# Performance work log

Hardware: AMD Instinct MI355X
Metric: run time of the kernel (lower is better)

## Reference

```python
import jax, jax.numpy as jnp
import numpy as np

B, T, H, NH, L = 2, 2048, 1024, 16, 6
D = H // NH          # head dim = 64
FF = 4 * H           # MLP hidden = 4096
EPS = 1e-5           # torch LayerNorm default

CAUSAL = np.tril(np.ones((T, T), dtype=bool))  # [T,T] lower-triangular mask


def _ln(x, g, b):
    m = jnp.mean(x, axis=-1, keepdims=True)
    v = jnp.mean(jnp.square(x - m), axis=-1, keepdims=True)
    return (x - m) * jax.lax.rsqrt(v + EPS) * g + b


def _block(x, p):
    Wq, bq, Wk, bk, Wv, bv, Wp, bp, W1, b1, W2, b2, g1, be1, g2, be2 = p
    mask = jnp.asarray(CAUSAL)
    # qkv projections -> [B, NH, T, D]
    q = (x @ Wq + bq).reshape(B, T, NH, D).transpose(0, 2, 1, 3)
    k = (x @ Wk + bk).reshape(B, T, NH, D).transpose(0, 2, 1, 3)
    v = (x @ Wv + bv).reshape(B, T, NH, D).transpose(0, 2, 1, 3)
    scores = jnp.einsum('bhtd,bhsd->bhts', q, k) / jnp.sqrt(jnp.float32(D))
    scores = jnp.where(mask, scores, -jnp.inf)
    attn = jax.nn.softmax(scores, axis=-1)
    o = jnp.einsum('bhts,bhsd->bhtd', attn, v)
    o = o.transpose(0, 2, 1, 3).reshape(B, T, H) @ Wp + bp
    x = _ln(x + o, g1, be1)            # residual then ln1 (post-LN, as in source)
    h = jax.nn.gelu(x @ W1 + b1, approximate=False)
    x = _ln(x + h @ W2 + b2, g2, be2)  # residual then ln2
    return x


def setup_inputs() -> dict:
    key = jax.random.key(0)
    ks = jax.random.split(key, 8)
    s = 0.02
    w = lambda k, shape: jax.random.normal(k, shape, jnp.float32) * s
    return {
        'x':  jax.random.normal(ks[0], (B, T, H), jnp.float32),
        'Wq': w(ks[1], (L, H, H)),  'bq': jnp.zeros((L, H), jnp.float32),
        'Wk': w(ks[2], (L, H, H)),  'bk': jnp.zeros((L, H), jnp.float32),
        'Wv': w(ks[3], (L, H, H)),  'bv': jnp.zeros((L, H), jnp.float32),
        'Wp': w(ks[4], (L, H, H)),  'bp': jnp.zeros((L, H), jnp.float32),
        'W1': w(ks[5], (L, H, FF)), 'b1': jnp.zeros((L, FF), jnp.float32),
        'W2': w(ks[6], (L, FF, H)), 'b2': jnp.zeros((L, H), jnp.float32),
        'g1': jnp.ones((L, H), jnp.float32),  'be1': jnp.zeros((L, H), jnp.float32),
        'g2': jnp.ones((L, H), jnp.float32),  'be2': jnp.zeros((L, H), jnp.float32),
    }


def reference(x, Wq, bq, Wk, bk, Wv, bv, Wp, bp, W1, b1, W2, b2, g1, be1, g2, be2):
    params = (Wq, bq, Wk, bk, Wv, bv, Wp, bp, W1, b1, W2, b2, g1, be1, g2, be2)
    y, _ = jax.lax.scan(lambda c, p: (_block(c, p), None), x, params)
    return y
```

## Files before the change

### kernel.cpp

```cpp
#include <hip/hip_runtime.h>

constexpr int cB  = 2;
constexpr int cT  = 2048;
constexpr int cH  = 1024;
constexpr int cNH = 16;
constexpr int cFF = 4096;
constexpr int cL  = 6;
constexpr int cM  = cB * cT;

typedef __attribute__((ext_vector_type(8))) short short8;
typedef __attribute__((ext_vector_type(4))) float f32x4;
typedef __attribute__((ext_vector_type(4))) unsigned short u16x4;
typedef unsigned short u16;

__device__ __forceinline__ u16 f2bf(float f) {
  union { float f; unsigned int u; } v; v.f = f;
  unsigned int u = v.u;
  return (u16)((u + 0x7fffu + ((u >> 16) & 1u)) >> 16);
}

__device__ __forceinline__ void glds16(const void* g, void* l) {
  __builtin_amdgcn_global_load_lds(
      (__attribute__((address_space(1))) void*)(unsigned long long)g,
      (__attribute__((address_space(3))) void*)(unsigned int)(unsigned long long)l,
      16, 0, 0);
}

#define EPI_F32 0
#define EPI_GELU 1
#define EPI_QKV 2

template <int EPI>
__global__ __launch_bounds__(512, 2) void gemm256(
    const u16* __restrict__ A,
    const u16* __restrict__ B0, const u16* __restrict__ B1, const u16* __restrict__ B2,
    const float* __restrict__ bias0, const float* __restrict__ bias1, const float* __restrict__ bias2,
    void* __restrict__ out0, void* __restrict__ out1, void* __restrict__ out2, void* __restrict__ out3,
    int M, int N, int K, int ntn)
{
  __shared__ u16 lds[65536];

  const int tid = threadIdx.x;
  const int wave = tid >> 6, lane = tid & 63;
  const int l15 = lane & 15, q4 = lane >> 4;
  const int wm = wave >> 2, wn = wave & 3;
  const int mt = blockIdx.x;
  const int by = blockIdx.y;
  const int mat = by / ntn;
  const int nt = by - mat * ntn;
  const u16* BT = (mat == 0) ? B0 : ((mat == 1) ? B1 : B2);
  const float* bias = (mat == 0) ? bias0 : ((mat == 1) ? bias1 : bias2);
  void* out = (mat == 0) ? out0 : ((mat == 1) ? out1 : out2);

  const int kz = blockIdx.z;
  const int kpc = K / gridDim.z;
  const int kb0 = kz * kpc;
  if (EPI == EPI_F32) {
    void* outs[4] = {out0, out1, out2, out3};
    out = outs[kz];
    if (kz > 0) bias = nullptr;
  }
  const int nkt = kpc >> 5;

  const u16* Ag[2]; const u16* Bg[2];
#pragma unroll
  for (int j = 0; j < 2; ++j) {
    const int d = j * 8192 + tid * 16;
    const int l = d ^ (((d >> 6) & 3) << 4);
    const int srow = l >> 6, skel = (l & 63) >> 1;
    Ag[j] = A  + (size_t)(mt * 256 + srow) * K + kb0 + skel;
    Bg[j] = BT + (size_t)(nt * 256 + srow) * K + kb0 + skel;
  }

  auto stageA = [&](int tt) {
    u16* dst = lds + ((tt & 3) << 14) + (tid << 3);
    glds16(Ag[0] + (tt << 5), dst);
    glds16(Ag[1] + (tt << 5), dst + 4096);
  };
  auto stageB = [&](int tt) {
    u16* dst = lds + ((tt & 3) << 14) + 8192 + (tid << 3);
    glds16(Bg[0] + (tt << 5), dst);
    glds16(Bg[1] + (tt << 5), dst + 4096);
  };

  const int sb = (l15 & 3) << 4;

  f32x4 acc[8][4] = {};
  short8 a[4], b[4];

  stageA(0); stageB(0); stageA(1); stageB(1);
  asm volatile("s_waitcnt vmcnt(4)" ::: "memory");
  __builtin_amdgcn_s_barrier();

  for (int t = 0; t < nkt; ++t) {
    const u16* As = lds + ((t & 3) << 14);
    const u16* Bs = As + 8192;
    const bool pre = (t + 2 < nkt);

#pragma unroll
    for (int nf = 0; nf < 4; ++nf) {
      const int r = wn * 64 + nf * 16 + l15;
      b[nf] = *(const short8*)(Bs + ((((r << 6) + (q4 << 4)) ^ sb) >> 1));
    }
#pragma unroll
    for (int m = 0; m < 4; ++m) {
      const int r = wm * 128 + m * 16 + l15;
      a[m] = *(const short8*)(As + ((((r << 6) + (q4 << 4)) ^ sb) >> 1));
    }
    if (pre) stageA(t + 2);
    __builtin_amdgcn_s_barrier();
    asm volatile("s_waitcnt lgkmcnt(0)" ::: "memory");
    __builtin_amdgcn_sched_barrier(0);
    __builtin_amdgcn_s_setprio(1);
#pragma unroll
    for (int m = 0; m < 4; ++m)
#pragma unroll
      for (int nf = 0; nf < 4; ++nf)
        acc[m][nf] = __builtin_amdgcn_mfma_f32_16x16x32_bf16(a[m], b[nf], acc[m][nf], 0, 0, 0);
    __builtin_amdgcn_s_setprio(0);
    __builtin_amdgcn_s_barrier();

#pragma unroll
    for (int m = 0; m < 4; ++m) {
      const int r = wm * 128 + (m + 4) * 16 + l15;
      a[m] = *(const short8*)(As + ((((r << 6) + (q4 << 4)) ^ sb) >> 1));
    }
    if (pre) stageB(t + 2);
    __builtin_amdgcn_s_barrier();
    asm volatile("s_waitcnt lgkmcnt(0)" ::: "memory");
    __builtin_amdgcn_sched_barrier(0);
    __builtin_amdgcn_s_setprio(1);
#pragma unroll
    for (int m = 0; m < 4; ++m)
#pragma unroll
      for (int nf = 0; nf < 4; ++nf)
        acc[m + 4][nf] = __builtin_amdgcn_mfma_f32_16x16x32_bf16(a[m], b[nf], acc[m + 4][nf], 0, 0, 0);
    __builtin_amdgcn_s_setprio(0);
    if (pre) asm volatile("s_waitcnt vmcnt(4)" ::: "memory");
    else     asm volatile("s_waitcnt vmcnt(0)" ::: "memory");
    __builtin_amdgcn_s_barrier();
  }

  float bj[4];
#pragma unroll
  for (int nf = 0; nf < 4; ++nf)
    bj[nf] = bias ? bias[nt * 256 + wn * 64 + nf * 16 + l15] : 0.0f;

  const float qscale = (EPI == EPI_QKV && mat == 0) ? 0.125f : 1.0f;

#pragma unroll
  for (int mf = 0; mf < 8; ++mf) {
#pragma unroll
    for (int nf = 0; nf < 4; ++nf) {
      const int n = nt * 256 + wn * 64 + nf * 16 + l15;
#pragma unroll
      for (int r = 0; r < 4; ++r) {
        const int m = mt * 256 + wm * 128 + mf * 16 + (q4 << 2) + r;
        float vv = acc[mf][nf][r] + bj[nf];
        if (EPI == EPI_F32) {
          ((float*)out)[(size_t)m * N + n] = vv;
        } else if (EPI == EPI_GELU) {
          float gg = vv * 0.5f * (1.0f + erff(vv * 0.70710678118654752f));
          ((u16*)out)[(size_t)m * N + n] = f2bf(gg);
        } else {
          const int bb = m >> 11, tt = m & (cT - 1);
          const int h = n >> 6, d = n & 63;
          ((u16*)out)[((((size_t)bb * cNH + h) * cT + tt) << 6) + d] = f2bf(vv * qscale);
        }
      }
    }
  }
}

template <int EPI>
__global__ __launch_bounds__(256) void gemm_bt(
    const u16* __restrict__ A,
    const u16* __restrict__ B0, const u16* __restrict__ B1, const u16* __restrict__ B2,
    const float* __restrict__ bias0, const float* __restrict__ bias1, const float* __restrict__ bias2,
    void* __restrict__ out0, void* __restrict__ out1, void* __restrict__ out2, void* __restrict__ out3,
    int M, int N, int K, int ntn)
{
  __shared__ u16 As[128 * 32];
  __shared__ u16 Bs[128 * 32];
  const int tid = threadIdx.x;
  const int wave = tid >> 6;
  const int lane = tid & 63;
  const int l15 = lane & 15;
  const int q4 = lane >> 4;
  const int mt = blockIdx.x;
  const int by = blockIdx.y;
  const int mat = by / ntn;
  const int nt = by - mat * ntn;
  const u16* BT = (mat == 0) ? B0 : ((mat == 1) ? B1 : B2);
  const float* bias = (mat == 0) ? bias0 : ((mat == 1) ? bias1 : bias2);
  void* out = (mat == 0) ? out0 : ((mat == 1) ? out1 : out2);

  const int kz = blockIdx.z;
  const int kpc = K / gridDim.z;
  const int kb0 = kz * kpc, kb1 = kb0 + kpc;
  if (EPI == EPI_F32) {
    void* outs[4] = {out0, out1, out2, out3};
    out = outs[kz];
    if (kz > 0) bias = nullptr;
  }

  const int wr = (wave >> 1) << 6;
  const int wc = (wave & 1) << 6;

  f32x4 acc[4][4] = {};

  const int srow = (wave << 5) + (lane >> 2);
  const int scol = (lane & 3) << 3;
  const u16* Ag = A + (size_t)(mt * 128 + srow) * K + scol;
  const u16* Bg = BT + (size_t)(nt * 128 + srow) * K + scol;
  u16* AsD = As + (wave << 10);
  u16* BsD = Bs + (wave << 10);

  for (int k0 = kb0; k0 < kb1; k0 += 32) {
    glds16(Ag + k0, AsD);
    glds16(Ag + k0 + 16 * K, AsD + 512);
    glds16(Bg + k0, BsD);
    glds16(Bg + k0 + 16 * K, BsD + 512);
    __syncthreads();
    short8 av[4], bv[4];
#pragma unroll
    for (int i = 0; i < 4; ++i)
      av[i] = *(const short8*)(As + ((wr + i * 16 + l15) << 5) + (q4 << 3));
#pragma unroll
    for (int j = 0; j < 4; ++j)
      bv[j] = *(const short8*)(Bs + ((wc + j * 16 + l15) << 5) + (q4 << 3));
#pragma unroll
    for (int i = 0; i < 4; ++i)
#pragma unroll
      for (int j = 0; j < 4; ++j)
        acc[i][j] = __builtin_amdgcn_mfma_f32_16x16x32_bf16(av[i], bv[j], acc[i][j], 0, 0, 0);
    __syncthreads();
  }

  float bj[4];
#pragma unroll
  for (int j = 0; j < 4; ++j) bj[j] = bias ? bias[nt * 128 + wc + j * 16 + l15] : 0.0f;

  const float qscale = (EPI == EPI_QKV && mat == 0) ? 0.125f : 1.0f;

#pragma unroll
  for (int i = 0; i < 4; ++i) {
#pragma unroll
    for (int j = 0; j < 4; ++j) {
      const int n = nt * 128 + wc + j * 16 + l15;
#pragma unroll
      for (int r = 0; r < 4; ++r) {
        const int m = mt * 128 + wr + i * 16 + (q4 << 2) + r;
        float vv = acc[i][j][r] + bj[j];
        if (EPI == EPI_F32) {
          ((float*)out)[(size_t)m * N + n] = vv;
        } else if (EPI == EPI_GELU) {
          float gg = vv * 0.5f * (1.0f + erff(vv * 0.70710678118654752f));
          ((u16*)out)[(size_t)m * N + n] = f2bf(gg);
        } else {
          const int b = m >> 11, t = m & (cT - 1);
          const int h = n >> 6, d = n & 63;
          ((u16*)out)[((((size_t)b * cNH + h) * cT + t) << 6) + d] = f2bf(vv * qscale);
        }
      }
    }
  }
}

__global__ __launch_bounds__(256) void flash_attn(
    const u16* __restrict__ q, const u16* __restrict__ k,
    const u16* __restrict__ v, u16* __restrict__ o)
{
  __shared__ u16 Vt[2][64 * 80];
  __shared__ u16 Pl[8][16 * 80];

  const int tid = threadIdx.x, wave = tid >> 6, lane = tid & 63;
  const int l15 = lane & 15, q4 = lane >> 4;
  const int bx = blockIdx.x;
  const int qtH = 31 - bx;
  const int qtL = bx;
  const int bh = blockIdx.y;
  const u16* qh = q + ((size_t)bh * cT << 6);
  const u16* kh = k + ((size_t)bh * cT << 6);
  const u16* vh = v + ((size_t)bh * cT << 6);

  short8 qfH[2], qfL[2];
#pragma unroll
  for (int kk = 0; kk < 2; ++kk) {
    qfH[kk] = *(const short8*)(qh + (size_t)((qtH << 6) + wave * 16 + l15) * 64 + kk * 32 + q4 * 8);
    qfL[kk] = *(const short8*)(qh + (size_t)((qtL << 6) + wave * 16 + l15) * 64 + kk * 32 + q4 * 8);
  }

  short8 ones;
#pragma unroll
  for (int i = 0; i < 8; ++i) ones[i] = (short)0x3F80;

  uint4 vs0, vs1;
  auto vload = [&](int st) {
    const int s0 = st << 6;
    const u16* src = vh + (size_t)(s0 + lane) * 64 + wave * 8;
    vs0 = *(const uint4*)(src);
    vs1 = *(const uint4*)(src + 32);
  };
  auto vwrite = [&](int buf) {
    u16* Vb = &Vt[buf][0];
    const int s = lane;
#pragma unroll
    for (int rd = 0; rd < 2; ++rd) {
      const int d0 = wave * 8 + rd * 32;
      uint4 vv = rd ? vs1 : vs0;
      Vb[(d0 + 0) * 80 + s] = (u16)(vv.x & 0xffff);
      Vb[(d0 + 1) * 80 + s] = (u16)(vv.x >> 16);
      Vb[(d0 + 2) * 80 + s] = (u16)(vv.y & 0xffff);
      Vb[(d0 + 3) * 80 + s] = (u16)(vv.y >> 16);
      Vb[(d0 + 4) * 80 + s] = (u16)(vv.z & 0xffff);
      Vb[(d0 + 5) * 80 + s] = (u16)(vv.z >> 16);
      Vb[(d0 + 6) * 80 + s] = (u16)(vv.w & 0xffff);
      Vb[(d0 + 7) * 80 + s] = (u16)(vv.w >> 16);
    }
  };

  auto loadK = [&](int st, short8* kf) {
    const int s0 = st << 6;
#pragma unroll
    for (int j = 0; j < 4; ++j)
#pragma unroll
      for (int kk = 0; kk < 2; ++kk)
        kf[j * 2 + kk] = *(const short8*)(kh + (size_t)(s0 + j * 16 + l15) * 64 + kk * 32 + q4 * 8);
  };

  f32x4 oaH[4] = {}, oaL[4] = {};
  f32x4 lsH = {}, lsL = {};

  auto tileQ = [&](int kt, int qt, const short8* qf, const short8* kf,
                   f32x4* oa, f32x4& ls, int buf, u16* pl) {
    f32x4 sa[4];
#pragma unroll
    for (int j = 0; j < 4; ++j) {
      f32x4 zz = {};
      zz = __builtin_amdgcn_mfma_f32_16x16x32_bf16(qf[0], kf[j * 2 + 0], zz, 0, 0, 0);
      zz = __builtin_amdgcn_mfma_f32_16x16x32_bf16(qf[1], kf[j * 2 + 1], zz, 0, 0, 0);
      sa[j] = zz;
    }
    if (kt == qt) {
#pragma unroll
      for (int r = 0; r < 4; ++r) {
        const int trow = wave * 16 + q4 * 4 + r;
#pragma unroll
        for (int j = 0; j < 4; ++j) {
          float pv = (j * 16 + l15 > trow) ? 0.0f : __expf(sa[j][r]);
          pl[(q4 * 4 + r) * 80 + j * 16 + l15] = f2bf(pv);
        }
      }
    } else {
#pragma unroll
      for (int r = 0; r < 4; ++r)
#pragma unroll
        for (int j = 0; j < 4; ++j)
          pl[(q4 * 4 + r) * 80 + j * 16 + l15] = f2bf(__expf(sa[j][r]));
    }
#pragma unroll
    for (int kk = 0; kk < 2; ++kk) {
      short8 pf = *(const short8*)(&pl[l15 * 80 + kk * 32 + q4 * 8]);
      ls = __builtin_amdgcn_mfma_f32_16x16x32_bf16(pf, ones, ls, 0, 0, 0);
#pragma unroll
      for (int jd = 0; jd < 4; ++jd) {
        short8 vf = *(const short8*)(&Vt[buf][(jd * 16 + l15) * 80 + kk * 32 + q4 * 8]);
        oa[jd] = __builtin_amdgcn_mfma_f32_16x16x32_bf16(pf, vf, oa[jd], 0, 0, 0);
      }
    }
  };

  auto tile = [&](int kt, const short8* kf, int buf) {
    tileQ(kt, qtH, qfH, kf, oaH, lsH, buf, &Pl[wave][0]);
    if (kt <= qtL)
      tileQ(kt, qtL, qfL, kf, oaL, lsL, buf, &Pl[wave + 4][0]);
  };

  const int nk = qtH + 1;
  short8 kfA[8], kfB[8];
  vload(0);
  loadK(0, kfA);
  vwrite(0);
  __syncthreads();

  int kt = 0;
  for (; kt + 2 <= nk; kt += 2) {
    vload(kt + 1);
    loadK(kt + 1, kfB);
    tile(kt, kfA, 0);
    vwrite(1);
    __syncthreads();
    if (kt + 2 < nk) { vload(kt + 2); loadK(kt + 2, kfA); }
    tile(kt + 1, kfB, 1);
    if (kt + 2 < nk) vwrite(0);
    __syncthreads();
  }
  if (kt < nk) { tile(kt, kfA, 0); }

  const int b = bh >> 4, h = bh & 15;
#pragma unroll
  for (int r = 0; r < 4; ++r) {
    const int tH = (qtH << 6) + wave * 16 + (q4 << 2) + r;
    const int tL = (qtL << 6) + wave * 16 + (q4 << 2) + r;
    const float invH = 1.0f / lsH[r];
    const float invL = 1.0f / lsL[r];
#pragma unroll
    for (int jd = 0; jd < 4; ++jd) {
      const int d = jd * 16 + l15;
      o[((size_t)(b * cT + tH)) * cH + (h << 6) + d] = f2bf(oaH[jd][r] * invH);
      o[((size_t)(b * cT + tL)) * cH + (h << 6) + d] = f2bf(oaL[jd][r] * invL);
    }
  }
}

template <int NY>
__global__ __launch_bounds__(256) void add_ln_k(
    const float* __restrict__ x,
    const float* __restrict__ y0, const float* __restrict__ y1,
    const float* __restrict__ y2, const float* __restrict__ y3,
    const float* __restrict__ g, const float* __restrict__ be,
    float* __restrict__ xout, u16* __restrict__ xb)
{
  const float* ys[4] = {y0, y1, y2, y3};
  const int row = blockIdx.x;
  const int c = threadIdx.x << 2;
  const size_t base = ((size_t)row << 10) + c;
  f32x4 vv = *(const f32x4*)(x + base);
#pragma unroll
  for (int p = 0; p < NY; ++p) {
    f32x4 yv = *(const f32x4*)(ys[p] + base);
#pragma unroll
    for (int t = 0; t < 4; ++t) vv[t] += yv[t];
  }
  float s1 = vv[0] + vv[1] + vv[2] + vv[3];
  float s2 = vv[0] * vv[0] + vv[1] * vv[1] + vv[2] * vv[2] + vv[3] * vv[3];
#pragma unroll
  for (int off = 1; off < 64; off <<= 1) {
    s1 += __shfl_xor(s1, off);
    s2 += __shfl_xor(s2, off);
  }
  __shared__ float sm[8];
  const int wave = threadIdx.x >> 6, lane = threadIdx.x & 63;
  if (lane == 0) { sm[wave] = s1; sm[wave + 4] = s2; }
  __syncthreads();
  const float S1 = sm[0] + sm[1] + sm[2] + sm[3];
  const float S2 = sm[4] + sm[5] + sm[6] + sm[7];
  const float mean = S1 * (1.0f / cH);
  const float var = S2 * (1.0f / cH) - mean * mean;
  const float rstd = rsqrtf(var + 1e-5f);
  f32x4 gv = *(const f32x4*)(g + c);
  f32x4 bv = *(const f32x4*)(be + c);
  f32x4 ov; u16x4 ob;
#pragma unroll
  for (int t = 0; t < 4; ++t) {
    ov[t] = (vv[t] - mean) * rstd * gv[t] + bv[t];
    ob[t] = f2bf(ov[t]);
  }
  *(f32x4*)(xout + base) = ov;
  *(u16x4*)(xb + base) = ob;
}

__global__ __launch_bounds__(256) void cvt_bf16(const float* __restrict__ in, u16* __restrict__ out)
{
  const size_t i = ((size_t)blockIdx.x * 256 + threadIdx.x) << 2;
  f32x4 vv = *(const f32x4*)(in + i);
  u16x4 ob;
#pragma unroll
  for (int t = 0; t < 4; ++t) ob[t] = f2bf(vv[t]);
  *(u16x4*)(out + i) = ob;
}

struct TransArgs {
  const float* src[6];
  u16* dst[6];
  int Kd[6];
  int Nd[6];
  int tofs[7];
};

__global__ __launch_bounds__(256) void transpose_w(TransArgs ta)
{
  __shared__ float tile[32][33];
  const int bid = blockIdx.x;
  int mi = 0;
#pragma unroll
  for (int i = 0; i < 5; ++i)
    if (bid >= ta.tofs[i + 1]) mi = i + 1;
  const int loc = bid - ta.tofs[mi];
  const int K = ta.Kd[mi], N = ta.Nd[mi];
  const int ntn = N >> 5;
  const int tk = loc / ntn, tn = loc - tk * ntn;
  const int r = threadIdx.x >> 3, c = (threadIdx.x & 7) << 2;
  f32x4 val = *(const f32x4*)(ta.src[mi] + (size_t)(tk * 32 + r) * N + tn * 32 + c);
#pragma unroll
  for (int t = 0; t < 4; ++t) tile[r][c + t] = val[t];
  __syncthreads();
  u16x4 ov;
#pragma unroll
  for (int t = 0; t < 4; ++t) ov[t] = f2bf(tile[c + t][r]);
  *(u16x4*)(ta.dst[mi] + (size_t)(tn * 32 + r) * K + tk * 32 + c) = ov;
}

extern "C" void kernel_launch(void* const* d_in, const int* in_sizes, int n_in,
                              void* d_out, int out_size, void* d_ws, size_t ws_size,
                              hipStream_t stream)
{
  const float* x_in = (const float*)d_in[0];
  const float* Wq = (const float*)d_in[1];
  const float* bq = (const float*)d_in[2];
  const float* Wk = (const float*)d_in[3];
  const float* bk = (const float*)d_in[4];
  const float* Wv = (const float*)d_in[5];
  const float* bv = (const float*)d_in[6];
  const float* Wp = (const float*)d_in[7];
  const float* bp = (const float*)d_in[8];
  const float* W1 = (const float*)d_in[9];
  const float* b1 = (const float*)d_in[10];
  const float* W2 = (const float*)d_in[11];
  const float* b2 = (const float*)d_in[12];
  const float* g1 = (const float*)d_in[13];
  const float* be1 = (const float*)d_in[14];
  const float* g2 = (const float*)d_in[15];
  const float* be2 = (const float*)d_in[16];

  char* w = (char*)d_ws;
  auto alloc = [&](size_t bytes) {
    char* p = w;
    w += (bytes + 255) & ~(size_t)255;
    return (void*)p;
  };
  float* xf = (float*)alloc((size_t)cM * cH * 4);
  u16* xb = (u16*)alloc((size_t)cM * cH * 2);
  u16* qb = (u16*)alloc((size_t)cM * cH * 2);
  u16* kb = (u16*)alloc((size_t)cM * cH * 2);
  u16* vb = (u16*)alloc((size_t)cM * cH * 2);
  u16* ob = (u16*)alloc((size_t)cM * cH * 2);
  u16* hb = (u16*)alloc((size_t)cM * cFF * 2);
  float* yb0 = (float*)alloc((size_t)cM * cH * 4);
  float* yb1 = (float*)alloc((size_t)cM * cH * 4);
  u16* wqT = (u16*)alloc((size_t)cH * cH * 2);
  u16* wkT = (u16*)alloc((size_t)cH * cH * 2);
  u16* wvT = (u16*)alloc((size_t)cH * cH * 2);
  u16* wpT = (u16*)alloc((size_t)cH * cH * 2);
  u16* w1T = (u16*)alloc((size_t)cH * cFF * 2);
  u16* w2T = (u16*)alloc((size_t)cH * cFF * 2);
  float* yb2 = (float*)qb;
  float* yb3 = (float*)vb;

  cvt_bf16<<<cM * cH / 1024, 256, 0, stream>>>(x_in, xb);
  const float* xcur = x_in;

  for (int l = 0; l < cL; ++l) {
    TransArgs ta;
    ta.src[0] = Wq + (size_t)l * cH * cH; ta.dst[0] = wqT; ta.Kd[0] = cH;  ta.Nd[0] = cH;
    ta.src[1] = Wk + (size_t)l * cH * cH; ta.dst[1] = wkT; ta.Kd[1] = cH;  ta.Nd[1] = cH;
    ta.src[2] = Wv + (size_t)l * cH * cH; ta.dst[2] = wvT; ta.Kd[2] = cH;  ta.Nd[2] = cH;
    ta.src[3] = Wp + (size_t)l * cH * cH; ta.dst[3] = wpT; ta.Kd[3] = cH;  ta.Nd[3] = cH;
    ta.src[4] = W1 + (size_t)l * cH * cFF; ta.dst[4] = w1T; ta.Kd[4] = cH;  ta.Nd[4] = cFF;
    ta.src[5] = W2 + (size_t)l * cFF * cH; ta.dst[5] = w2T; ta.Kd[5] = cFF; ta.Nd[5] = cH;
    ta.tofs[0] = 0;    ta.tofs[1] = 1024; ta.tofs[2] = 2048; ta.tofs[3] = 3072;
    ta.tofs[4] = 4096; ta.tofs[5] = 8192; ta.tofs[6] = 12288;
    transpose_w<<<12288, 256, 0, stream>>>(ta);

    gemm256<EPI_QKV><<<dim3(16, 12), 512, 0, stream>>>(
        xb, wqT, wkT, wvT, bq + l * cH, bk + l * cH, bv + l * cH,
        qb, kb, vb, nullptr, cM, cH, cH, 4);

    flash_attn<<<dim3(cT / 128, cB * cNH), 256, 0, stream>>>(qb, kb, vb, ob);

    gemm_bt<EPI_F32><<<dim3(32, 8, 2), 256, 0, stream>>>(
        ob, wpT, nullptr, nullptr, bp + l * cH, nullptr, nullptr,
        yb0, yb1, nullptr, nullptr, cM, cH, cH, 8);

    add_ln_k<2><<<cM, 256, 0, stream>>>(xcur, yb0, yb1, nullptr, nullptr,
                                        g1 + l * cH, be1 + l * cH, xf, xb);
    xcur = xf;

    gemm256<EPI_GELU><<<dim3(16, 16), 512, 0, stream>>>(
        xb, w1T, nullptr, nullptr, b1 + (size_t)l * cFF, nullptr, nullptr,
        hb, nullptr, nullptr, nullptr, cM, cFF, cH, 16);

    gemm256<EPI_F32><<<dim3(16, 4, 4), 512, 0, stream>>>(
        hb, w2T, nullptr, nullptr, b2 + l * cH, nullptr, nullptr,
        yb0, yb1, yb2, yb3, cM, cH, cFF, 4);

    float* xo = (l == cL - 1) ? (float*)d_out : xf;
    add_ln_k<4><<<cM, 256, 0, stream>>>(xcur, yb0, yb1, yb2, yb3,
                                        g2 + l * cH, be2 + l * cH, xo, xb);
  }
}
```

Before: 1.864 ms.

## Stage K tiles in LDS via direct global loads and swizzle attention LDS layouts

The flash attention kernel now stages K tiles into a double-buffered shared-memory buffer with global_load_lds, replacing per-wave register loads, and reads K fragments from LDS. It swaps the MFMA operand order so the score tile is transposed, letting each lane pack four probabilities with v_cvt_pk_bf16 into one 8-byte LDS store. The padded stride of 80 is replaced by an XOR-swizzled stride of 64, and the P scratch is shared between the high and low query tiles. This cuts VGPR pressure and redundant global K reads across waves. In exchange it adds LDS traffic and relies on the reused P buffer being safely ordered within each wave.

```diff
diff --git a/kernel.cpp b/kernel.cpp
--- a/kernel.cpp
+++ b/kernel.cpp
@@ -17,6 +17,12 @@
   union { float f; unsigned int u; } v; v.f = f;
   unsigned int u = v.u;
   return (u16)((u + 0x7fffu + ((u >> 16) & 1u)) >> 16);
+}
+
+__device__ __forceinline__ unsigned int cvt_pk_bf16(float lo, float hi) {
+  unsigned int r;
+  asm volatile("v_cvt_pk_bf16_f32 %0, %1, %2" : "=v"(r) : "v"(lo), "v"(hi));
+  return r;
 }
 
 __device__ __forceinline__ void glds16(const void* g, void* l) {
@@ -271,8 +277,9 @@
     const u16* __restrict__ q, const u16* __restrict__ k,
     const u16* __restrict__ v, u16* __restrict__ o)
 {
-  __shared__ u16 Vt[2][64 * 80];
-  __shared__ u16 Pl[8][16 * 80];
+  __shared__ u16 Ks[2][64 * 64];
+  __shared__ u16 Vt[2][64 * 64];
+  __shared__ u16 Pl[4][16 * 64];
 
   const int tid = threadIdx.x, wave = tid >> 6, lane = tid & 63;
   const int l15 = lane & 15, q4 = lane >> 4;
@@ -295,10 +302,22 @@
 #pragma unroll
   for (int i = 0; i < 8; ++i) ones[i] = (short)0x3F80;
 
+  const u16* kg[2];
+#pragma unroll
+  for (int r = 0; r < 2; ++r) {
+    const int d = tid * 16 + r * 4096;
+    const int l = d ^ (((d >> 7) & 7) << 4);
+    kg[r] = kh + (size_t)(l >> 7) * 64 + ((l & 127) >> 1);
+  }
+  auto stageK = [&](int st, int buf) {
+    u16* dst = &Ks[buf][0] + tid * 8;
+    glds16(kg[0] + (st << 12), dst);
+    glds16(kg[1] + (st << 12), dst + 2048);
+  };
+
   uint4 vs0, vs1;
   auto vload = [&](int st) {
-    const int s0 = st << 6;
-    const u16* src = vh + (size_t)(s0 + lane) * 64 + wave * 8;
+    const u16* src = vh + (size_t)((st << 6) + lane) * 64 + wave * 8;
     vs0 = *(const uint4*)(src);
     vs1 = *(const uint4*)(src + 32);
   };
@@ -309,94 +328,88 @@
     for (int rd = 0; rd < 2; ++rd) {
       const int d0 = wave * 8 + rd * 32;
       uint4 vv = rd ? vs1 : vs0;
-      Vb[(d0 + 0) * 80 + s] = (u16)(vv.x & 0xffff);
-      Vb[(d0 + 1) * 80 + s] = (u16)(vv.x >> 16);
-      Vb[(d0 + 2) * 80 + s] = (u16)(vv.y & 0xffff);
-      Vb[(d0 + 3) * 80 + s] = (u16)(vv.y >> 16);
-      Vb[(d0 + 4) * 80 + s] = (u16)(vv.z & 0xffff);
-      Vb[(d0 + 5) * 80 + s] = (u16)(vv.z >> 16);
-      Vb[(d0 + 6) * 80 + s] = (u16)(vv.w & 0xffff);
-      Vb[(d0 + 7) * 80 + s] = (u16)(vv.w >> 16);
-    }
-  };
-
-  auto loadK = [&](int st, short8* kf) {
-    const int s0 = st << 6;
-#pragma unroll
-    for (int j = 0; j < 4; ++j)
-#pragma unroll
-      for (int kk = 0; kk < 2; ++kk)
-        kf[j * 2 + kk] = *(const short8*)(kh + (size_t)(s0 + j * 16 + l15) * 64 + kk * 32 + q4 * 8);
+      const unsigned int x[4] = {vv.x, vv.y, vv.z, vv.w};
+#pragma unroll
+      for (int e2 = 0; e2 < 4; ++e2) {
+        const int da = d0 + e2 * 2, db = da + 1;
+        Vb[(da * 64 + s) ^ ((da & 7) << 3)] = (u16)(x[e2] & 0xffff);
+        Vb[(db * 64 + s) ^ ((db & 7) << 3)] = (u16)(x[e2] >> 16);
+      }
+    }
   };
 
   f32x4 oaH[4] = {}, oaL[4] = {};
   f32x4 lsH = {}, lsL = {};
 
-  auto tileQ = [&](int kt, int qt, const short8* qf, const short8* kf,
-                   f32x4* oa, f32x4& ls, int buf, u16* pl) {
+  const int sw = (l15 & 7) << 3;
+
+  auto tileQ = [&](int kt, int qt, const short8* qf, f32x4* oa, f32x4& ls, int buf) {
+    const u16* ks = &Ks[buf][0];
     f32x4 sa[4];
 #pragma unroll
     for (int j = 0; j < 4; ++j) {
+      const int rb = (j * 16 + l15) << 6;
+      short8 kf0 = *(const short8*)(ks + ((rb + q4 * 8) ^ sw));
+      short8 kf1 = *(const short8*)(ks + ((rb + 32 + q4 * 8) ^ sw));
       f32x4 zz = {};
-      zz = __builtin_amdgcn_mfma_f32_16x16x32_bf16(qf[0], kf[j * 2 + 0], zz, 0, 0, 0);
-      zz = __builtin_amdgcn_mfma_f32_16x16x32_bf16(qf[1], kf[j * 2 + 1], zz, 0, 0, 0);
+      zz = __builtin_amdgcn_mfma_f32_16x16x32_bf16(kf0, qf[0], zz, 0, 0, 0);
+      zz = __builtin_amdgcn_mfma_f32_16x16x32_bf16(kf1, qf[1], zz, 0, 0, 0);
       sa[j] = zz;
     }
-    if (kt == qt) {
+    u16* pl = &Pl[wave][0];
+    const int qrow = wave * 16 + l15;
+    const bool diag = (kt == qt);
+#pragma unroll
+    for (int j = 0; j < 4; ++j) {
+      float p[4];
 #pragma unroll
       for (int r = 0; r < 4; ++r) {
-        const int trow = wave * 16 + q4 * 4 + r;
-#pragma unroll
-        for (int j = 0; j < 4; ++j) {
-          float pv = (j * 16 + l15 > trow) ? 0.0f : __expf(sa[j][r]);
-          pl[(q4 * 4 + r) * 80 + j * 16 + l15] = f2bf(pv);
-        }
+        const int kv = j * 16 + q4 * 4 + r;
+        p[r] = (diag && kv > qrow) ? 0.0f : __expf(sa[j][r]);
       }
-    } else {
-#pragma unroll
-      for (int r = 0; r < 4; ++r)
-#pragma unroll
-        for (int j = 0; j < 4; ++j)
-          pl[(q4 * 4 + r) * 80 + j * 16 + l15] = f2bf(__expf(sa[j][r]));
+      uint2 wv;
+      wv.x = cvt_pk_bf16(p[0], p[1]);
+      wv.y = cvt_pk_bf16(p[2], p[3]);
+      *(uint2*)(pl + ((l15 * 64 + j * 16 + q4 * 4) ^ sw)) = wv;
     }
 #pragma unroll
     for (int kk = 0; kk < 2; ++kk) {
-      short8 pf = *(const short8*)(&pl[l15 * 80 + kk * 32 + q4 * 8]);
+      short8 pf = *(const short8*)(pl + ((l15 * 64 + kk * 32 + q4 * 8) ^ sw));
       ls = __builtin_amdgcn_mfma_f32_16x16x32_bf16(pf, ones, ls, 0, 0, 0);
 #pragma unroll
       for (int jd = 0; jd < 4; ++jd) {
-        short8 vf = *(const short8*)(&Vt[buf][(jd * 16 + l15) * 80 + kk * 32 + q4 * 8]);
+        const int dd = jd * 16 + l15;
+        short8 vf = *(const short8*)(&Vt[buf][(dd * 64 + kk * 32 + q4 * 8) ^ sw]);
         oa[jd] = __builtin_amdgcn_mfma_f32_16x16x32_bf16(pf, vf, oa[jd], 0, 0, 0);
       }
     }
   };
 
-  auto tile = [&](int kt, const short8* kf, int buf) {
-    tileQ(kt, qtH, qfH, kf, oaH, lsH, buf, &Pl[wave][0]);
+  auto tile = [&](int kt, int buf) {
+    tileQ(kt, qtH, qfH, oaH, lsH, buf);
     if (kt <= qtL)
-      tileQ(kt, qtL, qfL, kf, oaL, lsL, buf, &Pl[wave + 4][0]);
+      tileQ(kt, qtL, qfL, oaL, lsL, buf);
   };
 
   const int nk = qtH + 1;
-  short8 kfA[8], kfB[8];
+  stageK(0, 0);
   vload(0);
-  loadK(0, kfA);
   vwrite(0);
   __syncthreads();
 
   int kt = 0;
   for (; kt + 2 <= nk; kt += 2) {
+    stageK(kt + 1, 1);
     vload(kt + 1);
-    loadK(kt + 1, kfB);
-    tile(kt, kfA, 0);
+    tile(kt, 0);
     vwrite(1);
     __syncthreads();
-    if (kt + 2 < nk) { vload(kt + 2); loadK(kt + 2, kfA); }
-    tile(kt + 1, kfB, 1);
+    if (kt + 2 < nk) { stageK(kt + 2, 0); vload(kt + 2); }
+    tile(kt + 1, 1);
     if (kt + 2 < nk) vwrite(0);
     __syncthreads();
   }
-  if (kt < nk) { tile(kt, kfA, 0); }
+  if (kt < nk) { tile(kt, 0); }
 
   const int b = bh >> 4, h = bh & 15;
 #pragma unroll
```

Result: faster. 1.665 ms (-10.7%).
